# Optimization experiments

Measured on AMD Instinct MI355X. Metric: run time of the kernel, lower is better.

Reference implementation:

```python
import jax, jax.numpy as jnp
import numpy as np

B, S, D, H, HD = 8, 1374, 384, 6, 64
NUM_PATCHES = 1369  # (518 // 14) ** 2
NUM_PREFIX = 5      # 1 cls + 4 registers


def setup_inputs() -> dict:
    key = jax.random.key(0)
    ks = jax.random.split(key, 10)
    init = 0.02  # truncated_normal(0.02) approximated by scaled normal
    x = jax.random.normal(ks[0], (B, S, D), jnp.float32)
    wq = jax.random.truncated_normal(ks[1], -2.0, 2.0, (D, H, HD), jnp.float32) * init
    wk = jax.random.truncated_normal(ks[2], -2.0, 2.0, (D, H, HD), jnp.float32) * init
    wv = jax.random.truncated_normal(ks[3], -2.0, 2.0, (D, H, HD), jnp.float32) * init
    wo = jax.random.truncated_normal(ks[4], -2.0, 2.0, (H, HD, D), jnp.float32) * init
    bq = jnp.zeros((H, HD), jnp.float32)
    bk = jnp.zeros((H, HD), jnp.float32)
    bv = jnp.zeros((H, HD), jnp.float32)
    bo = jnp.zeros((D,), jnp.float32)
    keep_patch_indices = jax.random.randint(ks[5], (B, NUM_PATCHES), 0, NUM_PATCHES).astype(jnp.int64)
    return {"x": x, "wq": wq, "bq": bq, "wk": wk, "bk": bk, "wv": wv, "bv": bv,
            "wo": wo, "bo": bo, "keep_patch_indices": keep_patch_indices, "k_patches": 685}


def reference(x, wq, bq, wk, bk, wv, bv, wo, bo, keep_patch_indices, k_patches):
    # q/k/v projections: DenseGeneral to (heads, head_dim)
    q = jnp.einsum('bsd,dhe->bshe', x, wq) + bq
    k = jnp.einsum('bsd,dhe->bshe', x, wk) + bk
    v = jnp.einsum('bsd,dhe->bshe', x, wv) + bv

    z = jnp.einsum('bqhd,bkhd->bhqk', q / (HD ** 0.5), k)  # [B,H,S,S]
    attn_logits = z  # saved BEFORE masking (used by 'mse' criterion)

    # dynamic scatter mask: patch columns >= k_patches get -inf
    num_selected = keep_patch_indices.shape[1]
    patch_idx = jnp.arange(num_selected)
    indices_to_mask = jnp.where(patch_idx >= k_patches, patch_idx, num_selected) + NUM_PREFIX
    # out-of-bounds indices (== num_selected + NUM_PREFIX) are dropped by JAX scatter semantics
    z = z.at[:, :, :, indices_to_mask].set(-jnp.inf)

    attn_map = jax.nn.softmax(z, axis=-1)
    zo = jnp.einsum('bhqk,bkhd->bqhd', attn_map, v)
    output = jnp.einsum('bqhd,hdo->bqo', zo, wo) + bo  # wo contracts (heads, head_dim)

    # attn_aggregate = ['cls_token','reg_token','patch_token'], zoom_map_criterion='mse'
    am = attn_logits.mean(axis=1)  # mean over heads -> [B,S,S]
    aggs = jnp.stack([
        am[:, 0:1, :].mean(axis=1),      # cls token
        am[:, 1:5, :].mean(axis=1),      # register tokens
        am[:, 5:1374, :].mean(axis=1),   # patch tokens
    ], axis=1)                            # [B,3,S]
    attn_agg = aggs.mean(axis=1)          # [B,S]
    return output, attn_agg
```

## Files before the change

### kernel.cpp

```cpp
#include <hip/hip_runtime.h>
#include <stdint.h>

#define BB 8
#define SS 1374
#define DD 384
#define HH 6
#define HDIM 64
#define MROWS (BB*SS)
#define NPFX 5
#define SPAD 1376

typedef __attribute__((ext_vector_type(8))) short bf16x8;
typedef __attribute__((ext_vector_type(4))) float f32x4;
typedef __attribute__((ext_vector_type(4))) unsigned int u32x4;
typedef u32x4 __attribute__((aligned(4))) u32x4_u;

__device__ __forceinline__ unsigned short f2bf(float f){
  union { float f; unsigned int u; } v; v.f = f;
  return (unsigned short)((v.u + 0x7FFFu + ((v.u >> 16) & 1u)) >> 16);
}
__device__ __forceinline__ float bf2f(unsigned short b){
  union { float f; unsigned int u; } v; v.u = ((unsigned int)b) << 16; return v.f;
}
__device__ __forceinline__ unsigned int pk_bf16(float a, float b){
#if __has_builtin(__builtin_amdgcn_cvt_pk_bf16_f32)
  typedef __attribute__((ext_vector_type(2))) __bf16 bfv2;
  bfv2 p = __builtin_amdgcn_cvt_pk_bf16_f32(a, b);
  union { bfv2 v; unsigned int u; } c; c.v = p; return c.u;
#else
  return (unsigned int)f2bf(a) | ((unsigned int)f2bf(b) << 16);
#endif
}

__device__ __forceinline__ int xcd_remap(int i, int n){
  int q = n >> 3, r = n & 7;
  int x = i & 7, j = i >> 3;
  return (x < r ? x*(q+1) : r*(q+1) + (x - r)*q) + j;
}

__global__ void k_prep(const float* __restrict__ x, const float* __restrict__ wq,
                       const float* __restrict__ wk, const float* __restrict__ wv,
                       const float* __restrict__ wo,
                       unsigned short* __restrict__ xb, float* __restrict__ xpart,
                       unsigned short* __restrict__ wbT, unsigned short* __restrict__ woT){
  int bid = blockIdx.x, t = threadIdx.x;
  if (bid < 688){
    int b = bid / 86, ch = bid % 86;
    int d = t;
    int s0 = ch*16, s1 = s0 + 16; if (s1 > SS) s1 = SS;
    for (int s = s0; s < s1; ++s)
      xb[((size_t)b*SS + s)*DD + d] = f2bf(x[((size_t)b*SS + s)*DD + d]);
  } else if (bid < 752){
    int ib = bid - 688;
    int b = ib >> 3, c = ib & 7;
    int d = t;
    int s0 = c*172, s1 = s0 + 172; if (s1 > SS) s1 = SS;
    float acc = 0.f;
    for (int s = s0; s < s1; ++s){
      float w = (s == 0) ? (1.f/3.f) : (s < 5) ? (1.f/12.f) : (1.f/4107.f);
      acc += w * x[((size_t)b*SS + s)*DD + d];
    }
    xpart[(c*8 + b)*384 + d] = acc;
  } else {
    if (t >= 256) return;
    __shared__ float tile[32][33];
    int bid2 = bid - 752;
    int m = bid2 / 144, tl = bid2 % 144;
    int tr = tl / 12, tc = tl % 12;
    const float* src = (m==0) ? wq : (m==1) ? wk : (m==2) ? wv : wo;
    unsigned short* dst = (m < 3) ? (wbT + (size_t)m*384*384) : woT;
    int c = t & 31, r0 = t >> 5;
    #pragma unroll
    for (int p = 0; p < 4; ++p){
      int r = p*8 + r0;
      tile[r][c] = src[(size_t)(tr*32 + r)*384 + tc*32 + c];
    }
    __syncthreads();
    #pragma unroll
    for (int p = 0; p < 4; ++p){
      int r = p*8 + r0;
      dst[(size_t)(tc*32 + r)*384 + tr*32 + c] = f2bf(tile[c][r]);
    }
  }
}

template<int MODE>
__global__ __launch_bounds__(256) void k_gemm(
    const unsigned short* __restrict__ A, const unsigned short* __restrict__ Bt,
    const float* __restrict__ b0, const float* __restrict__ b1, const float* __restrict__ b2,
    unsigned short* __restrict__ qg, unsigned short* __restrict__ kgp,
    unsigned short* __restrict__ vt, float* __restrict__ out,
    const int* __restrict__ kpat, const float* __restrict__ xpart,
    const float* __restrict__ wqf, float* __restrict__ agg6, float* __restrict__ oagg)
{
  const int NT = (MODE==0) ? 18 : 6;
  int wg = xcd_remap(blockIdx.x, 86*NT);
  int mt = wg / NT, nt = wg % NT;
  const int t = threadIdx.x;
  const int w = t >> 6, lane = t & 63, quad = lane >> 4, l16 = lane & 15;
  const int wm = w >> 1, wn = w & 1;
  const int m0 = mt*128, n0 = nt*64;

  if (MODE == 0 && nt >= 12){
    int s0r_ = m0 % SS;
    int SKv = NPFX + kpat[0]; if (SKv > SS) SKv = SS; if (SKv < 1) SKv = 1;
    int lo = (SKv + 63) & ~63;
    if (s0r_ >= lo && s0r_ + 127 < SS) return;
  }

  constexpr int SMEM_SH = (MODE==0) ? 13824 : 17408;
  __shared__ unsigned short smem[SMEM_SH];
  unsigned short* As = smem;
  unsigned short* Bs = smem + 9216;
  f32x4 acc[4][2];
  #pragma unroll
  for (int i=0;i<4;i++){ acc[i][0] = (f32x4){0,0,0,0}; acc[i][1] = (f32x4){0,0,0,0}; }

  const int ar = t >> 1, akb = (t & 1) * 32;
  int ga = m0 + ar; if (ga > MROWS-1) ga = MROWS-1;
  const unsigned short* ap = A + (size_t)ga*384 + akb;
  const int br = t >> 2, bkb = (t & 3) * 16;
  const unsigned short* bp = Bt + (size_t)(n0 + br)*384 + bkb;

  u32x4 ra[4], rb[2];
  #pragma unroll
  for (int i=0;i<4;i++) ra[i] = *(const u32x4*)(ap + i*8);
  rb[0] = *(const u32x4*)(bp); rb[1] = *(const u32x4*)(bp + 8);

  for (int kc = 0; kc < 6; ++kc){
    asm volatile("s_waitcnt lgkmcnt(0)" ::: "memory");
    __builtin_amdgcn_s_barrier();
    #pragma unroll
    for (int i=0;i<4;i++) *(u32x4*)(As + ar*72 + akb + i*8) = ra[i];
    *(u32x4*)(Bs + br*72 + bkb)     = rb[0];
    *(u32x4*)(Bs + br*72 + bkb + 8) = rb[1];
    asm volatile("s_waitcnt lgkmcnt(0)" ::: "memory");
    __builtin_amdgcn_s_barrier();
    if (kc + 1 < 6){
      int kn = (kc+1)*64;
      #pragma unroll
      for (int i=0;i<4;i++) ra[i] = *(const u32x4*)(ap + kn + i*8);
      rb[0] = *(const u32x4*)(bp + kn); rb[1] = *(const u32x4*)(bp + kn + 8);
    }
    #pragma unroll
    for (int kh = 0; kh < 2; ++kh){
      bf16x8 af[4], bfr[2];
      #pragma unroll
      for (int rf = 0; rf < 4; ++rf)
        af[rf] = *(const bf16x8*)(As + (wm*64 + rf*16 + l16)*72 + kh*32 + quad*8);
      #pragma unroll
      for (int cf = 0; cf < 2; ++cf)
        bfr[cf] = *(const bf16x8*)(Bs + (wn*32 + cf*16 + l16)*72 + kh*32 + quad*8);
      #pragma unroll
      for (int rf = 0; rf < 4; ++rf)
        #pragma unroll
        for (int cf = 0; cf < 2; ++cf)
          acc[rf][cf] = __builtin_amdgcn_mfma_f32_16x16x32_bf16(af[rf], bfr[cf], acc[rf][cf], 0,0,0);
    }
  }

  const int b0r = m0 / SS, s0r = m0 % SS;
  __syncthreads();
  if (MODE == 1){
    float* CsF = (float*)smem;
    #pragma unroll
    for (int cf = 0; cf < 2; ++cf){
      int e = wn*32 + cf*16 + l16;
      float bias = b0[n0 + e];
      #pragma unroll
      for (int rf = 0; rf < 4; ++rf){
        int rr = wm*64 + rf*16 + quad*4;
        #pragma unroll
        for (int r4 = 0; r4 < 4; ++r4)
          CsF[(rr + r4)*68 + e] = acc[rf][cf][r4] + bias;
      }
    }
    __syncthreads();
    #pragma unroll
    for (int p = 0; p < 8; ++p){
      int r = p*16 + (t >> 4), c = t & 15;
      int rr = m0 + r;
      if (rr < MROWS){
        f32x4 v = *(const f32x4*)(CsF + r*68 + c*4);
        *(f32x4*)(out + (size_t)rr*384 + n0 + c*4) = v;
      }
    }
    if (nt == 0 && t < 128){
      int rr = m0 + t;
      if (rr < MROWS){
        float s = 0.f;
        #pragma unroll
        for (int hh = 0; hh < 6; ++hh) s += agg6[hh*MROWS + rr];
        oagg[rr] = s * (1.f/48.f);
      }
    }
  } else {
    const int mat = nt / 6, h = nt - mat*6;
    const float* bvp = (mat==0) ? b0 : (mat==1) ? b1 : b2;
    const float vsc = (mat==0) ? 0.125f : 1.f;
    if (mat < 2){
      unsigned short* Cs = As;
      unsigned short* dst = (mat==0) ? qg : kgp;
      float* xbl = (float*)Bs;
      float* qbl = ((float*)Bs) + 768;
      const int bb1 = (b0r + 1 < BB) ? b0r + 1 : BB - 1;
      #pragma unroll
      for (int cf = 0; cf < 2; ++cf){
        int e = wn*32 + cf*16 + l16;
        float bias = bvp[h*64 + e];
        #pragma unroll
        for (int rf = 0; rf < 4; ++rf){
          int rr = wm*64 + rf*16 + quad*4;
          #pragma unroll
          for (int r4 = 0; r4 < 4; ++r4)
            Cs[(rr + r4)*72 + e] = f2bf((acc[rf][cf][r4] + bias)*vsc);
        }
      }
      if (mat == 1){
        for (int i = t; i < 768; i += 256){
          int bbx = i / 384, d = i - bbx*384;
          int bsel = bbx ? bb1 : b0r;
          float s = 0.f;
          #pragma unroll
          for (int c8 = 0; c8 < 8; ++c8) s += xpart[(c8*8 + bsel)*384 + d];
          xbl[bbx*384 + d] = s;
        }
      }
      __syncthreads();
      if (mat == 1 && t < 128){
        int bbx = t >> 6, e = t & 63;
        float a = b0[h*64 + e];
        for (int d = 0; d < 384; ++d) a += xbl[bbx*384 + d] * wqf[(size_t)d*384 + h*64 + e];
        qbl[bbx*64 + e] = a;
      }
      if (mat == 1) __syncthreads();
      #pragma unroll
      for (int p = 0; p < 4; ++p){
        int r = p*32 + (t >> 3), c = t & 7;
        int rr = m0 + r;
        if (rr < MROWS){
          int s = s0r + r, bb = b0r;
          int bbx = 0;
          if (s >= SS){ s -= SS; ++bb; bbx = 1; }
          u32x4 v = *(const u32x4*)(Cs + r*72 + c*8);
          *(u32x4*)(dst + (((size_t)(bb*HH + h))*SS + s)*64 + c*8) = v;
          if (mat == 1){
            const float* qh = qbl + bbx*64 + c*8;
            float part = 0.f;
            #pragma unroll
            for (int j = 0; j < 4; ++j){
              unsigned int u = v[j];
              part += qh[2*j]     * bf2f((unsigned short)(u & 0xFFFFu));
              part += qh[2*j + 1] * bf2f((unsigned short)(u >> 16));
            }
            part += __shfl_xor(part, 1);
            part += __shfl_xor(part, 2);
            part += __shfl_xor(part, 4);
            if (c == 0) agg6[h*MROWS + rr] = part;
          }
        }
      }
    } else {
      unsigned short* CsV = As;
      #pragma unroll
      for (int cf = 0; cf < 2; ++cf){
        int e = wn*32 + cf*16 + l16;
        float bias = bvp[h*64 + e];
        #pragma unroll
        for (int rf = 0; rf < 4; ++rf){
          int rr = wm*64 + rf*16 + quad*4;
          #pragma unroll
          for (int p = 0; p < 2; ++p)
            *(unsigned int*)(CsV + e*136 + rr + p*2) =
                pk_bf16(acc[rf][cf][p*2] + bias, acc[rf][cf][p*2+1] + bias);
        }
      }
      __syncthreads();
      const bool nowrap = (s0r + 127 < SS) && (m0 + 127 < MROWS);
      if (nowrap){
        int e = t >> 2;
        unsigned short* vrow = vt + ((size_t)(b0r*HH + h)*64 + e)*SPAD + s0r;
        #pragma unroll
        for (int i = 0; i < 4; ++i){
          int c = (t & 3)*4 + i;
          u32x4 v = *(const u32x4*)(CsV + e*136 + c*8);
          *(u32x4_u*)(vrow + c*8) = v;
        }
      } else {
        for (int idx = t; idx < 64*64; idx += 256){
          int e = idx >> 6, sp = (idx & 63)*2;
          int rr = m0 + sp;
          if (rr < MROWS){
            int s = s0r + sp, bb = b0r;
            if (s >= SS){ s -= SS; ++bb; }
            *(unsigned int*)(vt + ((size_t)(bb*HH + h)*64 + e)*SPAD + s) =
                *(const unsigned int*)(CsV + e*136 + sp);
          }
        }
      }
    }
  }
}

#define KSTR 72
__global__ __launch_bounds__(256) void k_attn(
    const unsigned short* __restrict__ qg, const unsigned short* __restrict__ kg,
    const unsigned short* __restrict__ vt, unsigned short* __restrict__ zo,
    const int* __restrict__ kpat)
{
  const int NQB = 22;
  int wg = xcd_remap(blockIdx.x, 48*NQB);
  int qb = wg % NQB, bh = wg / NQB;
  int t = threadIdx.x, w = t >> 6, lane = t & 63, quad = lane >> 4, l16 = lane & 15;
  int SK = NPFX + kpat[0]; if (SK > SS) SK = SS; if (SK < 1) SK = 1;
  int niter = (SK + 63) >> 6;
  __shared__ unsigned short Ks[2][64*KSTR];
  __shared__ unsigned short Vs[2][64*KSTR];
  __shared__ unsigned short Ps[4][16*KSTR];
  unsigned short* Pw = &Ps[w][0];
  int q0 = qb*64 + w*16;

  bf16x8 aq[2];
  {
    int qrow = q0 + l16; if (qrow > SS-1) qrow = SS-1;
    const unsigned short* p = qg + ((size_t)bh*SS + qrow)*64;
    aq[0] = *(const bf16x8*)(p + quad*8);
    aq[1] = *(const bf16x8*)(p + 32 + quad*8);
  }
  f32x4 o[4];
  float rsum[4] = {0.f,0.f,0.f,0.f};
  #pragma unroll
  for (int i=0;i<4;i++) o[i] = (f32x4){0.f,0.f,0.f,0.f};

  const int srow = t >> 2, sc = (t & 3) * 16;
  const unsigned short* kbase = kg + ((size_t)bh*SS)*64;
  const unsigned short* vbase = vt + ((size_t)bh*64)*SPAD;
  u32x4 rk[2], rv[2];
  {
    rk[0] = *(const u32x4*)(kbase + (size_t)srow*64 + sc);
    rk[1] = *(const u32x4*)(kbase + (size_t)srow*64 + sc + 8);
    rv[0] = *(const u32x4*)(vbase + (size_t)srow*SPAD + sc);
    rv[1] = *(const u32x4*)(vbase + (size_t)srow*SPAD + sc + 8);
  }

  for (int it = 0; it < niter; ++it){
    int k0 = it*64;
    int cur = it & 1;
    unsigned short* Ksc = &Ks[cur][0];
    unsigned short* Vsc = &Vs[cur][0];
    *(u32x4*)(Ksc + srow*KSTR + sc)     = rk[0];
    *(u32x4*)(Ksc + srow*KSTR + sc + 8) = rk[1];
    *(u32x4*)(Vsc + srow*KSTR + sc)     = rv[0];
    *(u32x4*)(Vsc + srow*KSTR + sc + 8) = rv[1];
    if (it + 1 < niter){
      int kn = k0 + 64;
      int krow = kn + srow; if (krow > SS-1) krow = SS-1;
      rk[0] = *(const u32x4*)(kbase + (size_t)krow*64 + sc);
      rk[1] = *(const u32x4*)(kbase + (size_t)krow*64 + sc + 8);
      rv[0] = *(const u32x4*)(vbase + (size_t)srow*SPAD + kn + sc);
      rv[1] = *(const u32x4*)(vbase + (size_t)srow*SPAD + kn + sc + 8);
    }
    asm volatile("s_waitcnt lgkmcnt(0)" ::: "memory");
    __builtin_amdgcn_s_barrier();

    bool tail = (k0 + 64 > SK);
    #pragma unroll
    for (int ks = 0; ks < 2; ++ks){
      float pp[2][4];
      bf16x8 bkf[2][2];
      #pragma unroll
      for (int ns = 0; ns < 2; ++ns)
        #pragma unroll
        for (int ec = 0; ec < 2; ++ec)
          bkf[ns][ec] = *(const bf16x8*)(Ksc + (ks*32 + 2*l16 + ns)*KSTR + ec*32 + quad*8);
      __builtin_amdgcn_s_setprio(1);
      f32x4 z0 = (f32x4){0.f,0.f,0.f,0.f};
      f32x4 z1 = (f32x4){0.f,0.f,0.f,0.f};
      z0 = __builtin_amdgcn_mfma_f32_16x16x32_bf16(aq[0], bkf[0][0], z0, 0,0,0);
      z0 = __builtin_amdgcn_mfma_f32_16x16x32_bf16(aq[1], bkf[0][1], z0, 0,0,0);
      z1 = __builtin_amdgcn_mfma_f32_16x16x32_bf16(aq[0], bkf[1][0], z1, 0,0,0);
      z1 = __builtin_amdgcn_mfma_f32_16x16x32_bf16(aq[1], bkf[1][1], z1, 0,0,0);
      __builtin_amdgcn_s_setprio(0);
      bool v0 = !tail || (k0 + ks*32 + 2*l16)     < SK;
      bool v1 = !tail || (k0 + ks*32 + 2*l16 + 1) < SK;
      #pragma unroll
      for (int rg = 0; rg < 4; ++rg){
        pp[0][rg] = v0 ? __expf(z0[rg]) : 0.f;
        pp[1][rg] = v1 ? __expf(z1[rg]) : 0.f;
      }
      #pragma unroll
      for (int rg = 0; rg < 4; ++rg){
        rsum[rg] += pp[0][rg] + pp[1][rg];
        *(unsigned int*)(Pw + (quad*4 + rg)*KSTR + ks*32 + 2*l16) =
            pk_bf16(pp[0][rg], pp[1][rg]);
      }
    }
    #pragma unroll
    for (int kc = 0; kc < 2; ++kc){
      bf16x8 ap = *(const bf16x8*)(Pw + l16*KSTR + kc*32 + quad*8);
      __builtin_amdgcn_s_setprio(1);
      #pragma unroll
      for (int nc = 0; nc < 4; ++nc){
        bf16x8 vf = *(const bf16x8*)(Vsc + (nc*16 + l16)*KSTR + kc*32 + quad*8);
        o[nc] = __builtin_amdgcn_mfma_f32_16x16x32_bf16(ap, vf, o[nc], 0,0,0);
      }
      __builtin_amdgcn_s_setprio(0);
    }
  }
  int b = bh / HH, h = bh - (bh/HH)*HH;
  #pragma unroll
  for (int rg = 0; rg < 4; ++rg){
    float s = rsum[rg];
    #pragma unroll
    for (int off = 8; off >= 1; off >>= 1) s += __shfl_xor(s, off);
    int q = q0 + quad*4 + rg;
    if (q >= SS) continue;
    float inv = 1.f / s;
    unsigned short* dst = zo + ((size_t)b*SS + q)*384 + h*64;
    #pragma unroll
    for (int nc = 0; nc < 4; ++nc) dst[nc*16 + l16] = f2bf(o[nc][rg]*inv);
  }
}

extern "C" void kernel_launch(void* const* d_in, const int* in_sizes, int n_in,
                              void* d_out, int out_size, void* d_ws, size_t ws_size,
                              hipStream_t stream){
  const float* x  = (const float*)d_in[0];
  const float* wq = (const float*)d_in[1];
  const float* bq = (const float*)d_in[2];
  const float* wk = (const float*)d_in[3];
  const float* bk = (const float*)d_in[4];
  const float* wv = (const float*)d_in[5];
  const float* bv = (const float*)d_in[6];
  const float* wo = (const float*)d_in[7];
  const float* bo = (const float*)d_in[8];
  const int* kpat = (const int*)d_in[10];
  float* out = (float*)d_out;
  float* out_agg = out + (size_t)MROWS*DD;

  char* ws = (char*)d_ws;
  unsigned short* xb  = (unsigned short*)(ws);
  unsigned short* wbT = (unsigned short*)(ws +  8441856);
  unsigned short* woT = (unsigned short*)(ws +  9326592);
  unsigned short* qg  = (unsigned short*)(ws +  9621504);
  unsigned short* kg  = (unsigned short*)(ws + 18063360);
  unsigned short* vt  = (unsigned short*)(ws + 26505216);
  unsigned short* zo  = (unsigned short*)(ws + 34959360);
  float* xpart        = (float*)(ws + 43401216);
  float* agg6         = (float*)(ws + 43499520);
  (void)in_sizes; (void)n_in; (void)out_size; (void)ws_size;

  k_prep<<<1328, 384, 0, stream>>>(x, wq, wk, wv, wo, xb, xpart, wbT, woT);
  k_gemm<0><<<86*18, 256, 0, stream>>>(xb, wbT, bq, bk, bv, qg, kg, vt, nullptr, kpat, xpart, wq, agg6, nullptr);
  k_attn<<<48*22, 256, 0, stream>>>(qg, kg, vt, zo, kpat);
  k_gemm<1><<<86*6, 256, 0, stream>>>(zo, woT, bo, nullptr, nullptr, nullptr, nullptr, nullptr, out, nullptr, nullptr, nullptr, agg6, out_agg);
}
```

Measured before the change: 197.1 us.

## Precompute per-batch query mean in a separate kernel and vectorize x conversion

Moves the per-batch weighted-mean query projection out of every K-tile GEMM block into a small k_qbar kernel, so it is computed once per batch rather than redundantly in each block. k_prep now fuses the x bf16 conversion with the partial weighted sums, uses 256 threads and float4 loads with packed bf16 stores, and drops the separate reduction blocks. In exchange there is one extra kernel launch and xpart grows to 86 chunks that k_qbar must reduce.

```diff
diff --git a/kernel.cpp b/kernel.cpp
--- a/kernel.cpp
+++ b/kernel.cpp
@@ -12,6 +12,7 @@
 
 typedef __attribute__((ext_vector_type(8))) short bf16x8;
 typedef __attribute__((ext_vector_type(4))) float f32x4;
+typedef __attribute__((ext_vector_type(2))) unsigned int u32x2;
 typedef __attribute__((ext_vector_type(4))) unsigned int u32x4;
 typedef u32x4 __attribute__((aligned(4))) u32x4_u;
 
@@ -38,33 +39,52 @@
   return (x < r ? x*(q+1) : r*(q+1) + (x - r)*q) + j;
 }
 
-__global__ void k_prep(const float* __restrict__ x, const float* __restrict__ wq,
-                       const float* __restrict__ wk, const float* __restrict__ wv,
-                       const float* __restrict__ wo,
-                       unsigned short* __restrict__ xb, float* __restrict__ xpart,
-                       unsigned short* __restrict__ wbT, unsigned short* __restrict__ woT){
+__global__ __launch_bounds__(256) void k_prep(const float* __restrict__ x,
+    const float* __restrict__ wq, const float* __restrict__ wk, const float* __restrict__ wv,
+    const float* __restrict__ wo, unsigned short* __restrict__ xb, float* __restrict__ xpart,
+    unsigned short* __restrict__ wbT, unsigned short* __restrict__ woT){
   int bid = blockIdx.x, t = threadIdx.x;
   if (bid < 688){
     int b = bid / 86, ch = bid % 86;
-    int d = t;
-    int s0 = ch*16, s1 = s0 + 16; if (s1 > SS) s1 = SS;
-    for (int s = s0; s < s1; ++s)
-      xb[((size_t)b*SS + s)*DD + d] = f2bf(x[((size_t)b*SS + s)*DD + d]);
-  } else if (bid < 752){
-    int ib = bid - 688;
-    int b = ib >> 3, c = ib & 7;
-    int d = t;
-    int s0 = c*172, s1 = s0 + 172; if (s1 > SS) s1 = SS;
-    float acc = 0.f;
-    for (int s = s0; s < s1; ++s){
-      float w = (s == 0) ? (1.f/3.f) : (s < 5) ? (1.f/12.f) : (1.f/4107.f);
-      acc += w * x[((size_t)b*SS + s)*DD + d];
-    }
-    xpart[(c*8 + b)*384 + d] = acc;
+    int s0 = ch*16;
+    const float* xrow = x + ((size_t)b*SS + s0)*DD;
+    unsigned short* xrowb = xb + ((size_t)b*SS + s0)*DD;
+    if (s0 + 16 <= SS){
+      #pragma unroll
+      for (int p = 0; p < 6; ++p){
+        int fl = p*1024 + t*4;
+        f32x4 v = *(const f32x4*)(xrow + fl);
+        u32x2 st = { pk_bf16(v[0], v[1]), pk_bf16(v[2], v[3]) };
+        *(u32x2*)(xrowb + fl) = st;
+      }
+    } else {
+      #pragma unroll
+      for (int p = 0; p < 6; ++p){
+        int fl = p*1024 + t*4;
+        if (s0 + fl/384 < SS){
+          f32x4 v = *(const f32x4*)(xrow + fl);
+          u32x2 st = { pk_bf16(v[0], v[1]), pk_bf16(v[2], v[3]) };
+          *(u32x2*)(xrowb + fl) = st;
+        }
+      }
+    }
+    float acc0 = 0.f, acc1 = 0.f;
+    int d1 = t + 256;
+    #pragma unroll
+    for (int i = 0; i < 16; ++i){
+      int s = s0 + i;
+      if (s < SS){
+        float w = (s == 0) ? (1.f/3.f) : (s < 5) ? (1.f/12.f) : (1.f/4107.f);
+        acc0 += w * xrow[(size_t)i*DD + t];
+        if (t < 128) acc1 += w * xrow[(size_t)i*DD + d1];
+      }
+    }
+    float* xp = xpart + ((size_t)ch*8 + b)*384;
+    xp[t] = acc0;
+    if (t < 128) xp[d1] = acc1;
   } else {
-    if (t >= 256) return;
     __shared__ float tile[32][33];
-    int bid2 = bid - 752;
+    int bid2 = bid - 688;
     int m = bid2 / 144, tl = bid2 % 144;
     int tr = tl / 12, tc = tl % 12;
     const float* src = (m==0) ? wq : (m==1) ? wk : (m==2) ? wv : wo;
@@ -82,6 +102,29 @@
       dst[(size_t)(tc*32 + r)*384 + tr*32 + c] = f2bf(tile[c][r]);
     }
   }
+}
+
+__global__ __launch_bounds__(256) void k_qbar(const float* __restrict__ xpart,
+    const float* __restrict__ wq, const float* __restrict__ bq, float* __restrict__ qbar){
+  __shared__ float xs[DD];
+  __shared__ float red[256];
+  int b = blockIdx.x / 6, nc = blockIdx.x % 6;
+  int t = threadIdx.x;
+  for (int d = t; d < DD; d += 256){
+    float s = 0.f;
+    #pragma unroll 4
+    for (int ch = 0; ch < 86; ++ch) s += xpart[((size_t)ch*8 + b)*384 + d];
+    xs[d] = s;
+  }
+  __syncthreads();
+  int n = t & 63, kq = t >> 6;
+  float a = 0.f;
+  #pragma unroll 4
+  for (int d = kq*96; d < (kq+1)*96; ++d) a += xs[d] * wq[(size_t)d*384 + nc*64 + n];
+  red[t] = a;
+  __syncthreads();
+  if (t < 64)
+    qbar[b*384 + nc*64 + n] = red[n] + red[n+64] + red[n+128] + red[n+192] + bq[nc*64 + n];
 }
 
 template<int MODE>
@@ -90,8 +133,8 @@
     const float* __restrict__ b0, const float* __restrict__ b1, const float* __restrict__ b2,
     unsigned short* __restrict__ qg, unsigned short* __restrict__ kgp,
     unsigned short* __restrict__ vt, float* __restrict__ out,
-    const int* __restrict__ kpat, const float* __restrict__ xpart,
-    const float* __restrict__ wqf, float* __restrict__ agg6, float* __restrict__ oagg)
+    const int* __restrict__ kpat, const float* __restrict__ qbar,
+    float* __restrict__ agg6, float* __restrict__ oagg)
 {
   const int NT = (MODE==0) ? 18 : 6;
   int wg = xcd_remap(blockIdx.x, 86*NT);
@@ -201,9 +244,6 @@
     if (mat < 2){
       unsigned short* Cs = As;
       unsigned short* dst = (mat==0) ? qg : kgp;
-      float* xbl = (float*)Bs;
-      float* qbl = ((float*)Bs) + 768;
-      const int bb1 = (b0r + 1 < BB) ? b0r + 1 : BB - 1;
       #pragma unroll
       for (int cf = 0; cf < 2; ++cf){
         int e = wn*32 + cf*16 + l16;
@@ -216,36 +256,18 @@
             Cs[(rr + r4)*72 + e] = f2bf((acc[rf][cf][r4] + bias)*vsc);
         }
       }
-      if (mat == 1){
-        for (int i = t; i < 768; i += 256){
-          int bbx = i / 384, d = i - bbx*384;
-          int bsel = bbx ? bb1 : b0r;
-          float s = 0.f;
-          #pragma unroll
-          for (int c8 = 0; c8 < 8; ++c8) s += xpart[(c8*8 + bsel)*384 + d];
-          xbl[bbx*384 + d] = s;
-        }
-      }
       __syncthreads();
-      if (mat == 1 && t < 128){
-        int bbx = t >> 6, e = t & 63;
-        float a = b0[h*64 + e];
-        for (int d = 0; d < 384; ++d) a += xbl[bbx*384 + d] * wqf[(size_t)d*384 + h*64 + e];
-        qbl[bbx*64 + e] = a;
-      }
-      if (mat == 1) __syncthreads();
       #pragma unroll
       for (int p = 0; p < 4; ++p){
         int r = p*32 + (t >> 3), c = t & 7;
         int rr = m0 + r;
         if (rr < MROWS){
           int s = s0r + r, bb = b0r;
-          int bbx = 0;
-          if (s >= SS){ s -= SS; ++bb; bbx = 1; }
+          if (s >= SS){ s -= SS; ++bb; }
           u32x4 v = *(const u32x4*)(Cs + r*72 + c*8);
           *(u32x4*)(dst + (((size_t)(bb*HH + h))*SS + s)*64 + c*8) = v;
           if (mat == 1){
-            const float* qh = qbl + bbx*64 + c*8;
+            const float* qh = qbar + bb*384 + h*64 + c*8;
             float part = 0.f;
             #pragma unroll
             for (int j = 0; j < 4; ++j){
@@ -447,11 +469,13 @@
   unsigned short* vt  = (unsigned short*)(ws + 26505216);
   unsigned short* zo  = (unsigned short*)(ws + 34959360);
   float* xpart        = (float*)(ws + 43401216);
-  float* agg6         = (float*)(ws + 43499520);
+  float* qbar         = (float*)(ws + 44457984);
+  float* agg6         = (float*)(ws + 44470272);
   (void)in_sizes; (void)n_in; (void)out_size; (void)ws_size;
 
-  k_prep<<<1328, 384, 0, stream>>>(x, wq, wk, wv, wo, xb, xpart, wbT, woT);
-  k_gemm<0><<<86*18, 256, 0, stream>>>(xb, wbT, bq, bk, bv, qg, kg, vt, nullptr, kpat, xpart, wq, agg6, nullptr);
+  k_prep<<<1264, 256, 0, stream>>>(x, wq, wk, wv, wo, xb, xpart, wbT, woT);
+  k_qbar<<<48, 256, 0, stream>>>(xpart, wq, bq, qbar);
+  k_gemm<0><<<86*18, 256, 0, stream>>>(xb, wbT, bq, bk, bv, qg, kg, vt, nullptr, kpat, qbar, agg6, nullptr);
   k_attn<<<48*22, 256, 0, stream>>>(qg, kg, vt, zo, kpat);
-  k_gemm<1><<<86*6, 256, 0, stream>>>(zo, woT, bo, nullptr, nullptr, nullptr, nullptr, nullptr, out, nullptr, nullptr, nullptr, agg6, out_agg);
-}
+  k_gemm<1><<<86*6, 256, 0, stream>>>(zo, woT, bo, nullptr, nullptr, nullptr, nullptr, nullptr, out, nullptr, nullptr, agg6, out_agg);
+}
```

Result: faster. 191.8 us (-2.7%).
